# Performance work log

Measured on AMD Instinct MI355X. Metric: run time of the kernel, lower is better.

The kernel has to match this reference:

```python
import jax, jax.numpy as jnp
import numpy as np

DIM = 2048
N_HEADS = 16
HEAD_DIM = DIM // N_HEADS
B, S = 2, 2048


def apply_rotary(x, cos, sin):
    # x: [..., dim]; cos/sin broadcast to [..., dim//2]
    # even/odd interleaved rotation, matching the torch ::2 / 1::2 indexing
    xe = x[..., 0::2]
    xo = x[..., 1::2]
    oe = xe * cos - xo * sin
    oo = xo * cos + xe * sin
    return jnp.stack([oe, oo], axis=-1).reshape(x.shape)


def setup_inputs() -> dict:
    key = jax.random.key(0)
    ks = jax.random.split(key, 12)
    scale = 1.0 / np.sqrt(DIM)
    x = jax.random.normal(ks[0], (B, S, DIM), dtype=jnp.float32)
    cos = jax.random.normal(ks[1], (S, DIM // 2), dtype=jnp.float32)
    sin = jax.random.normal(ks[2], (S, DIM // 2), dtype=jnp.float32)
    mask = jnp.zeros((1, 1, S, S), dtype=jnp.float32)
    Wq = jax.random.normal(ks[3], (DIM, DIM), dtype=jnp.float32) * scale
    bq = jnp.zeros((DIM,), dtype=jnp.float32)
    Wk = jax.random.normal(ks[4], (DIM, DIM), dtype=jnp.float32) * scale
    bk = jnp.zeros((DIM,), dtype=jnp.float32)
    Wv = jax.random.normal(ks[5], (DIM, DIM), dtype=jnp.float32) * scale
    bv = jnp.zeros((DIM,), dtype=jnp.float32)
    Wo = jax.random.normal(ks[6], (DIM, DIM), dtype=jnp.float32) * scale
    bo = jnp.zeros((DIM,), dtype=jnp.float32)
    return {"x": x, "cos": cos, "sin": sin, "mask": mask,
            "Wq": Wq, "bq": bq, "Wk": Wk, "bk": bk,
            "Wv": Wv, "bv": bv, "Wo": Wo, "bo": bo}


def reference(x, cos, sin, mask, Wq, bq, Wk, bk, Wv, bv, Wo, bo):
    # Linear projections (torch nn.Linear: y = x @ W.T + b)
    q = jnp.einsum('bsd,ed->bse', x, Wq) + bq
    k = jnp.einsum('bsd,ed->bse', x, Wk) + bk
    v = jnp.einsum('bsd,ed->bse', x, Wv) + bv
    # RoPE on full dim, then split into heads (faithful to source ordering)
    q = apply_rotary(q, cos, sin).reshape(B, S, N_HEADS, HEAD_DIM)
    k = apply_rotary(k, cos, sin).reshape(B, S, N_HEADS, HEAD_DIM)
    v = v.reshape(B, S, N_HEADS, HEAD_DIM)
    scale = 1.0 / jnp.sqrt(jnp.float32(HEAD_DIM))
    attn = jnp.einsum('bqhd,bkhd->bhqk', q, k) * scale  # [B,H,S,S]
    attn = attn + mask
    attn = jax.nn.softmax(attn, axis=-1)
    out = jnp.einsum('bhqk,bkhd->bqhd', attn, v).reshape(B, S, DIM)
    return jnp.einsum('bsd,ed->bse', out, Wo) + bo
```

## Files before the change

kernel.cpp:

```cpp
#include <hip/hip_runtime.h>

#define DIM   2048
#define SLEN  2048
#define BATCH 2
#define NHEAD 16
#define HDIM  128
#define MROWS (BATCH*SLEN)

typedef __attribute__((ext_vector_type(8))) __bf16 bf16x8;
typedef __attribute__((ext_vector_type(4))) float  f32x4;
typedef __attribute__((ext_vector_type(8))) unsigned short u16x8;
typedef __attribute__((ext_vector_type(4))) unsigned short u16x4;

__device__ __forceinline__ unsigned short f2bf(float f) {
  union { float f; unsigned u; } v; v.f = f;
  unsigned r = v.u + 0x7FFFu + ((v.u >> 16) & 1u);
  return (unsigned short)(r >> 16);
}
__device__ __forceinline__ float bf2f(unsigned short h) {
  union { unsigned u; float f; } v; v.u = ((unsigned)h) << 16;
  return v.f;
}
__device__ __forceinline__ void gload16(const void* g, void* l) {
  __builtin_amdgcn_global_load_lds(
      (const __attribute__((address_space(1))) void*)g,
      (__attribute__((address_space(3))) void*)l, 16, 0, 0);
}

__global__ __launch_bounds__(256) void conv_f32_bf16(
    const float* __restrict__ in, unsigned short* __restrict__ out, int n4) {
  int t = blockIdx.x * 256 + threadIdx.x;
  if (t >= n4) return;
  f32x4 v = *(const f32x4*)(in + (size_t)t * 4);
  u16x4 o;
  o[0] = f2bf(v[0]); o[1] = f2bf(v[1]); o[2] = f2bf(v[2]); o[3] = f2bf(v[3]);
  *(u16x4*)(out + (size_t)t * 4) = o;
}

template<int OUT_MODE>
__global__ __launch_bounds__(256) void gemm_bt(
    const unsigned short* __restrict__ A,
    const unsigned short* __restrict__ Bw,
    const float* __restrict__ bias,
    void* __restrict__ Cout, int M, int N, int K)
{
  __shared__ __align__(16) unsigned short As[128][32];
  __shared__ __align__(16) unsigned short Bs[128][32];
  const int tid  = threadIdx.x;
  const int lane = tid & 63;
  const int wid  = tid >> 6;
  const int wr   = wid >> 1, wc = wid & 1;
  const int lrow = lane >> 4, lcol = lane & 15;
  const int row0 = blockIdx.x * 128, col0 = blockIdx.y * 128;

  f32x4 acc[4][4] = {};

  const unsigned short* Ablk = A  + (size_t)row0 * K;
  const unsigned short* Bblk = Bw + (size_t)col0 * K;
  char* AsB = (char*)&As[0][0];
  char* BsB = (char*)&Bs[0][0];

  for (int k0 = 0; k0 < K; k0 += 32) {
#pragma unroll
    for (int r = 0; r < 2; ++r) {
      int f = r * 256 + tid;
      gload16(Ablk + (size_t)(f >> 2) * K + k0 + (f & 3) * 8, AsB + (r * 256 + wid * 64) * 16);
      gload16(Bblk + (size_t)(f >> 2) * K + k0 + (f & 3) * 8, BsB + (r * 256 + wid * 64) * 16);
    }
    __syncthreads();
    bf16x8 af[4], bfv[4];
#pragma unroll
    for (int m = 0; m < 4; ++m)
      af[m] = *(const bf16x8*)&As[wr * 64 + m * 16 + lcol][lrow * 8];
#pragma unroll
    for (int n = 0; n < 4; ++n)
      bfv[n] = *(const bf16x8*)&Bs[wc * 64 + n * 16 + lcol][lrow * 8];
#pragma unroll
    for (int m = 0; m < 4; ++m)
#pragma unroll
      for (int n = 0; n < 4; ++n)
        acc[m][n] = __builtin_amdgcn_mfma_f32_16x16x32_bf16(af[m], bfv[n], acc[m][n], 0, 0, 0);
    __syncthreads();
  }

#pragma unroll
  for (int m = 0; m < 4; ++m) {
#pragma unroll
    for (int n = 0; n < 4; ++n) {
      int col = col0 + wc * 64 + n * 16 + lcol;
      float bv = bias[col];
      if (OUT_MODE == 2) {
        int row = row0 + wr * 64 + m * 16 + lrow * 4;
        u16x4 o;
#pragma unroll
        for (int j = 0; j < 4; ++j) o[j] = f2bf(acc[m][n][j] + bv);
        *(u16x4*)((unsigned short*)Cout +
                  ((size_t)((row >> 11) * DIM + col)) * SLEN + (row & (SLEN - 1))) = o;
      } else {
#pragma unroll
        for (int j = 0; j < 4; ++j) {
          int row = row0 + wr * 64 + m * 16 + lrow * 4 + j;
          float val = acc[m][n][j] + bv;
          if (OUT_MODE == 1) ((unsigned short*)Cout)[(size_t)row * N + col] = f2bf(val);
          else               ((float*)Cout)[(size_t)row * N + col] = val;
        }
      }
    }
  }
}

__global__ __launch_bounds__(256) void rope_inplace(
    unsigned short* __restrict__ q,
    const float* __restrict__ cosT, const float* __restrict__ sinT) {
  int t   = blockIdx.x * 256 + threadIdx.x;
  int row = t >> 8;
  int e0  = (t & 255) * 8;
  int s   = row & (SLEN - 1);
  unsigned short* p = q + (size_t)row * DIM + e0;
  u16x8 v = *(u16x8*)p;
  f32x4 c  = *(const f32x4*)(cosT + (size_t)s * (DIM / 2) + (e0 >> 1));
  f32x4 sn = *(const f32x4*)(sinT + (size_t)s * (DIM / 2) + (e0 >> 1));
#pragma unroll
  for (int i = 0; i < 4; ++i) {
    float xe = bf2f(v[2 * i]), xo = bf2f(v[2 * i + 1]);
    float oe = xe * c[i] - xo * sn[i];
    float oo = xo * c[i] + xe * sn[i];
    v[2 * i] = f2bf(oe); v[2 * i + 1] = f2bf(oo);
  }
  *(u16x8*)p = v;
}

__global__ __launch_bounds__(256) void attn_fwd(
    const unsigned short* __restrict__ Q,
    const unsigned short* __restrict__ Kg,
    const unsigned short* __restrict__ VtG,
    const float* __restrict__ mask,
    unsigned short* __restrict__ O)
{
  __shared__ __align__(16) unsigned short Ks[64][128];
  __shared__ __align__(16) unsigned short Vts[128][64];
  __shared__ __align__(16) unsigned short Ps[4][16][64];

  const int qt = blockIdx.x, h = blockIdx.y, b = blockIdx.z;
  const int tid = threadIdx.x, lane = tid & 63, wid = tid >> 6;
  const int lrow = lane >> 4, lcol = lane & 15;
  const int sx = (lcol & 7) << 4;
  const float scale = 0.08838834764831845f;

  const unsigned short* Qb  = Q  + ((size_t)(b * SLEN + qt * 64)) * DIM + h * HDIM;
  const unsigned short* Kb  = Kg + (size_t)(b * SLEN) * DIM + h * HDIM;
  const unsigned short* Vtb = VtG + ((size_t)(b * DIM + h * HDIM)) * SLEN;

  bf16x8 qf[4];
#pragma unroll
  for (int kk = 0; kk < 4; ++kk)
    qf[kk] = *(const bf16x8*)(Qb + (size_t)(wid * 16 + lcol) * DIM + kk * 32 + lrow * 8);

  float m_run[4], l_run[4];
  f32x4 acc_o[8] = {};
#pragma unroll
  for (int r = 0; r < 4; ++r) { m_run[r] = -1e30f; l_run[r] = 0.f; }

  char* KsB  = (char*)&Ks[0][0];
  char* VtsB = (char*)&Vts[0][0];
  char* PsB  = (char*)&Ps[0][0][0];

  for (int kt = 0; kt < SLEN / 64; ++kt) {
    __syncthreads();
#pragma unroll
    for (int r = 0; r < 4; ++r) {
      int L = r * 256 + wid * 64 + lane;
      int krow = L >> 4, kc = (L & 15) ^ (krow & 7);
      gload16(Kb + (size_t)(kt * 64 + krow) * DIM + kc * 8,
              KsB + (size_t)(r * 256 + wid * 64) * 16);
    }
#pragma unroll
    for (int r = 0; r < 4; ++r) {
      int L = r * 256 + wid * 64 + lane;
      int d = L >> 3, vc = (L & 7) ^ (d & 7);
      gload16(Vtb + (size_t)d * SLEN + kt * 64 + vc * 8,
              VtsB + (size_t)(r * 256 + wid * 64) * 16);
    }
    __syncthreads();

    f32x4 sacc[4] = {};
#pragma unroll
    for (int kn = 0; kn < 4; ++kn)
#pragma unroll
      for (int kk = 0; kk < 4; ++kk) {
        bf16x8 kf = *(const bf16x8*)(KsB + (size_t)(kn * 16 + lcol) * 256
                                         + ((kk * 64 + lrow * 16) ^ sx));
        sacc[kn] = __builtin_amdgcn_mfma_f32_16x16x32_bf16(qf[kk], kf, sacc[kn], 0, 0, 0);
      }

    int q0 = qt * 64 + wid * 16 + lrow * 4;
    float sv[4][4];
#pragma unroll
    for (int kn = 0; kn < 4; ++kn) {
      int kglob = kt * 64 + kn * 16 + lcol;
#pragma unroll
      for (int r = 0; r < 4; ++r)
        sv[kn][r] = sacc[kn][r] * scale + mask[(size_t)(q0 + r) * SLEN + kglob];
    }
    float alpha[4];
#pragma unroll
    for (int r = 0; r < 4; ++r) {
      float m0 = fmaxf(fmaxf(sv[0][r], sv[1][r]), fmaxf(sv[2][r], sv[3][r]));
#pragma unroll
      for (int off = 1; off < 16; off <<= 1) m0 = fmaxf(m0, __shfl_xor(m0, off, 64));
      float mt = fmaxf(m_run[r], m0);
      alpha[r] = __expf(m_run[r] - mt);
      m_run[r] = mt;
    }
    float pv[4][4];
#pragma unroll
    for (int r = 0; r < 4; ++r) {
      float rsum = 0.f;
#pragma unroll
      for (int kn = 0; kn < 4; ++kn) {
        float pe = __expf(sv[kn][r] - m_run[r]);
        pv[kn][r] = pe; rsum += pe;
      }
#pragma unroll
      for (int off = 1; off < 16; off <<= 1) rsum += __shfl_xor(rsum, off, 64);
      l_run[r] = l_run[r] * alpha[r] + rsum;
    }
#pragma unroll
    for (int d = 0; d < 8; ++d) {
      f32x4 t = acc_o[d];
      t[0] *= alpha[0]; t[1] *= alpha[1]; t[2] *= alpha[2]; t[3] *= alpha[3];
      acc_o[d] = t;
    }
#pragma unroll
    for (int kn = 0; kn < 4; ++kn)
#pragma unroll
      for (int r = 0; r < 4; ++r) {
        int prow = lrow * 4 + r;
        *(unsigned short*)(PsB + wid * 2048 + prow * 128
                           + ((kn * 32 + lcol * 2) ^ ((prow & 7) << 4))) = f2bf(pv[kn][r]);
      }

    bf16x8 pf[2];
#pragma unroll
    for (int ks = 0; ks < 2; ++ks)
      pf[ks] = *(const bf16x8*)(PsB + wid * 2048 + lcol * 128
                                + ((ks * 64 + lrow * 16) ^ sx));
#pragma unroll
    for (int d = 0; d < 8; ++d)
#pragma unroll
      for (int ks = 0; ks < 2; ++ks) {
        bf16x8 vf = *(const bf16x8*)(VtsB + (size_t)(d * 16 + lcol) * 128
                                          + ((ks * 64 + lrow * 16) ^ sx));
        acc_o[d] = __builtin_amdgcn_mfma_f32_16x16x32_bf16(pf[ks], vf, acc_o[d], 0, 0, 0);
      }
  }

  int orow0 = b * SLEN + qt * 64 + wid * 16 + lrow * 4;
#pragma unroll
  for (int d = 0; d < 8; ++d)
#pragma unroll
    for (int r = 0; r < 4; ++r) {
      float o = acc_o[d][r] / l_run[r];
      O[(size_t)(orow0 + r) * DIM + h * HDIM + d * 16 + lcol] = f2bf(o);
    }
}

extern "C" void kernel_launch(void* const* d_in, const int* in_sizes, int n_in,
                              void* d_out, int out_size, void* d_ws, size_t ws_size,
                              hipStream_t stream) {
  const float* x    = (const float*)d_in[0];
  const float* cosT = (const float*)d_in[1];
  const float* sinT = (const float*)d_in[2];
  const float* mask = (const float*)d_in[3];
  const float* Wq   = (const float*)d_in[4];
  const float* bq   = (const float*)d_in[5];
  const float* Wk   = (const float*)d_in[6];
  const float* bk   = (const float*)d_in[7];
  const float* Wv   = (const float*)d_in[8];
  const float* bv   = (const float*)d_in[9];
  const float* Wo   = (const float*)d_in[10];
  const float* bo   = (const float*)d_in[11];

  const size_t MB = 1u << 20;
  if (ws_size < 72 * MB) return;

  char* ws = (char*)d_ws;
  unsigned short* xb = (unsigned short*)(ws);
  unsigned short* qb = (unsigned short*)(ws + 16 * MB);
  unsigned short* kb = (unsigned short*)(ws + 32 * MB);
  unsigned short* Vt = (unsigned short*)(ws + 48 * MB);
  unsigned short* Wb = (unsigned short*)(ws + 64 * MB);
  unsigned short* Ob = xb;

  dim3 gGemm(MROWS / 128, DIM / 128);

  conv_f32_bf16<<<8192, 256, 0, stream>>>(x, xb, (MROWS * DIM) / 4);
  conv_f32_bf16<<<4096, 256, 0, stream>>>(Wq, Wb, (DIM * DIM) / 4);
  gemm_bt<1><<<gGemm, 256, 0, stream>>>(xb, Wb, bq, qb, MROWS, DIM, DIM);
  conv_f32_bf16<<<4096, 256, 0, stream>>>(Wk, Wb, (DIM * DIM) / 4);
  gemm_bt<1><<<gGemm, 256, 0, stream>>>(xb, Wb, bk, kb, MROWS, DIM, DIM);
  conv_f32_bf16<<<4096, 256, 0, stream>>>(Wv, Wb, (DIM * DIM) / 4);
  gemm_bt<2><<<gGemm, 256, 0, stream>>>(xb, Wb, bv, Vt, MROWS, DIM, DIM);
  rope_inplace<<<4096, 256, 0, stream>>>(qb, cosT, sinT);
  rope_inplace<<<4096, 256, 0, stream>>>(kb, cosT, sinT);
  attn_fwd<<<dim3(SLEN / 64, NHEAD, BATCH), 256, 0, stream>>>(qb, kb, Vt, mask, Ob);
  conv_f32_bf16<<<4096, 256, 0, stream>>>(Wo, Wb, (DIM * DIM) / 4);
  gemm_bt<0><<<gGemm, 256, 0, stream>>>(Ob, Wb, bo, d_out, MROWS, DIM, DIM);
}
```

Measured before the change: 450.7 us.

## Transpose score MFMA layout, fold scale into RoPE, lazy softmax rescaling

Swaps the MFMA operands for the QK^T product so each lane owns a single query row. This turns the softmax max and sum reductions into two cross-lane shuffles instead of four per row, and lets the mask be read as vectorized f32x4 loads. The 1/sqrt(d) scale moves into the Q RoPE kernel. The running-max rescale of the output accumulator is skipped unless some row's max rises by more than 8, trading a bounded growth of exp values for fewer multiplies. The P tile write layout is adjusted to match, and the final division becomes a reciprocal multiply.

```diff
diff --git a/kernel.cpp b/kernel.cpp
--- a/kernel.cpp
+++ b/kernel.cpp
@@ -111,7 +111,7 @@
 
 __global__ __launch_bounds__(256) void rope_inplace(
     unsigned short* __restrict__ q,
-    const float* __restrict__ cosT, const float* __restrict__ sinT) {
+    const float* __restrict__ cosT, const float* __restrict__ sinT, float scale) {
   int t   = blockIdx.x * 256 + threadIdx.x;
   int row = t >> 8;
   int e0  = (t & 255) * 8;
@@ -123,8 +123,8 @@
 #pragma unroll
   for (int i = 0; i < 4; ++i) {
     float xe = bf2f(v[2 * i]), xo = bf2f(v[2 * i + 1]);
-    float oe = xe * c[i] - xo * sn[i];
-    float oo = xo * c[i] + xe * sn[i];
+    float oe = (xe * c[i] - xo * sn[i]) * scale;
+    float oo = (xo * c[i] + xe * sn[i]) * scale;
     v[2 * i] = f2bf(oe); v[2 * i + 1] = f2bf(oo);
   }
   *(u16x8*)p = v;
@@ -145,21 +145,19 @@
   const int tid = threadIdx.x, lane = tid & 63, wid = tid >> 6;
   const int lrow = lane >> 4, lcol = lane & 15;
   const int sx = (lcol & 7) << 4;
-  const float scale = 0.08838834764831845f;
 
   const unsigned short* Qb  = Q  + ((size_t)(b * SLEN + qt * 64)) * DIM + h * HDIM;
   const unsigned short* Kb  = Kg + (size_t)(b * SLEN) * DIM + h * HDIM;
   const unsigned short* Vtb = VtG + ((size_t)(b * DIM + h * HDIM)) * SLEN;
+  const float* maskRow = mask + (size_t)(qt * 64 + wid * 16 + lcol) * SLEN;
 
   bf16x8 qf[4];
 #pragma unroll
   for (int kk = 0; kk < 4; ++kk)
     qf[kk] = *(const bf16x8*)(Qb + (size_t)(wid * 16 + lcol) * DIM + kk * 32 + lrow * 8);
 
-  float m_run[4], l_run[4];
+  float m_run = -1e30f, l_run = 0.f;
   f32x4 acc_o[8] = {};
-#pragma unroll
-  for (int r = 0; r < 4; ++r) { m_run[r] = -1e30f; l_run[r] = 0.f; }
 
   char* KsB  = (char*)&Ks[0][0];
   char* VtsB = (char*)&Vts[0][0];
@@ -190,55 +188,54 @@
       for (int kk = 0; kk < 4; ++kk) {
         bf16x8 kf = *(const bf16x8*)(KsB + (size_t)(kn * 16 + lcol) * 256
                                          + ((kk * 64 + lrow * 16) ^ sx));
-        sacc[kn] = __builtin_amdgcn_mfma_f32_16x16x32_bf16(qf[kk], kf, sacc[kn], 0, 0, 0);
+        sacc[kn] = __builtin_amdgcn_mfma_f32_16x16x32_bf16(kf, qf[kk], sacc[kn], 0, 0, 0);
       }
 
-    int q0 = qt * 64 + wid * 16 + lrow * 4;
-    float sv[4][4];
+    float sv[16];
 #pragma unroll
     for (int kn = 0; kn < 4; ++kn) {
-      int kglob = kt * 64 + kn * 16 + lcol;
+      f32x4 mv = *(const f32x4*)(maskRow + kt * 64 + kn * 16 + lrow * 4);
+#pragma unroll
+      for (int r = 0; r < 4; ++r) sv[kn * 4 + r] = sacc[kn][r] + mv[r];
+    }
+
+    float pmax = sv[0];
+#pragma unroll
+    for (int i = 1; i < 16; ++i) pmax = fmaxf(pmax, sv[i]);
+    pmax = fmaxf(pmax, __shfl_xor(pmax, 16, 64));
+    pmax = fmaxf(pmax, __shfl_xor(pmax, 32, 64));
+
+    if (!__all(pmax - m_run <= 8.0f)) {
+      float mnew = fmaxf(m_run, pmax);
+      float alpha = __expf(m_run - mnew);
+      m_run = mnew;
+      l_run *= alpha;
+      float ar[4];
+#pragma unroll
+      for (int r = 0; r < 4; ++r) ar[r] = __shfl(alpha, lrow * 4 + r, 64);
+#pragma unroll
+      for (int d = 0; d < 8; ++d) {
+        f32x4 t = acc_o[d];
+#pragma unroll
+        for (int r = 0; r < 4; ++r) t[r] *= ar[r];
+        acc_o[d] = t;
+      }
+    }
+
+    float pv[16];
+    float rsum = 0.f;
+#pragma unroll
+    for (int i = 0; i < 16; ++i) { float pe = __expf(sv[i] - m_run); pv[i] = pe; rsum += pe; }
+    rsum += __shfl_xor(rsum, 16, 64);
+    rsum += __shfl_xor(rsum, 32, 64);
+    l_run += rsum;
+
+#pragma unroll
+    for (int kn = 0; kn < 4; ++kn)
 #pragma unroll
       for (int r = 0; r < 4; ++r)
-        sv[kn][r] = sacc[kn][r] * scale + mask[(size_t)(q0 + r) * SLEN + kglob];
-    }
-    float alpha[4];
-#pragma unroll
-    for (int r = 0; r < 4; ++r) {
-      float m0 = fmaxf(fmaxf(sv[0][r], sv[1][r]), fmaxf(sv[2][r], sv[3][r]));
-#pragma unroll
-      for (int off = 1; off < 16; off <<= 1) m0 = fmaxf(m0, __shfl_xor(m0, off, 64));
-      float mt = fmaxf(m_run[r], m0);
-      alpha[r] = __expf(m_run[r] - mt);
-      m_run[r] = mt;
-    }
-    float pv[4][4];
-#pragma unroll
-    for (int r = 0; r < 4; ++r) {
-      float rsum = 0.f;
-#pragma unroll
-      for (int kn = 0; kn < 4; ++kn) {
-        float pe = __expf(sv[kn][r] - m_run[r]);
-        pv[kn][r] = pe; rsum += pe;
-      }
-#pragma unroll
-      for (int off = 1; off < 16; off <<= 1) rsum += __shfl_xor(rsum, off, 64);
-      l_run[r] = l_run[r] * alpha[r] + rsum;
-    }
-#pragma unroll
-    for (int d = 0; d < 8; ++d) {
-      f32x4 t = acc_o[d];
-      t[0] *= alpha[0]; t[1] *= alpha[1]; t[2] *= alpha[2]; t[3] *= alpha[3];
-      acc_o[d] = t;
-    }
-#pragma unroll
-    for (int kn = 0; kn < 4; ++kn)
-#pragma unroll
-      for (int r = 0; r < 4; ++r) {
-        int prow = lrow * 4 + r;
-        *(unsigned short*)(PsB + wid * 2048 + prow * 128
-                           + ((kn * 32 + lcol * 2) ^ ((prow & 7) << 4))) = f2bf(pv[kn][r]);
-      }
+        *(unsigned short*)(PsB + wid * 2048 + lcol * 128
+                           + ((kn * 32 + (lrow * 4 + r) * 2) ^ sx)) = f2bf(pv[kn * 4 + r]);
 
     bf16x8 pf[2];
 #pragma unroll
@@ -255,12 +252,15 @@
       }
   }
 
+  float linv[4];
+#pragma unroll
+  for (int r = 0; r < 4; ++r) linv[r] = 1.0f / __shfl(l_run, lrow * 4 + r, 64);
   int orow0 = b * SLEN + qt * 64 + wid * 16 + lrow * 4;
 #pragma unroll
   for (int d = 0; d < 8; ++d)
 #pragma unroll
     for (int r = 0; r < 4; ++r) {
-      float o = acc_o[d][r] / l_run[r];
+      float o = acc_o[d][r] * linv[r];
       O[(size_t)(orow0 + r) * DIM + h * HDIM + d * 16 + lcol] = f2bf(o);
     }
 }
@@ -293,6 +293,7 @@
   unsigned short* Ob = xb;
 
   dim3 gGemm(MROWS / 128, DIM / 128);
+  const float scale = 0.08838834764831845f;
 
   conv_f32_bf16<<<8192, 256, 0, stream>>>(x, xb, (MROWS * DIM) / 4);
   conv_f32_bf16<<<4096, 256, 0, stream>>>(Wq, Wb, (DIM * DIM) / 4);
@@ -301,8 +302,8 @@
   gemm_bt<1><<<gGemm, 256, 0, stream>>>(xb, Wb, bk, kb, MROWS, DIM, DIM);
   conv_f32_bf16<<<4096, 256, 0, stream>>>(Wv, Wb, (DIM * DIM) / 4);
   gemm_bt<2><<<gGemm, 256, 0, stream>>>(xb, Wb, bv, Vt, MROWS, DIM, DIM);
-  rope_inplace<<<4096, 256, 0, stream>>>(qb, cosT, sinT);
-  rope_inplace<<<4096, 256, 0, stream>>>(kb, cosT, sinT);
+  rope_inplace<<<4096, 256, 0, stream>>>(qb, cosT, sinT, scale);
+  rope_inplace<<<4096, 256, 0, stream>>>(kb, cosT, sinT, 1.0f);
   attn_fwd<<<dim3(SLEN / 64, NHEAD, BATCH), 256, 0, stream>>>(qb, kb, Vt, mask, Ob);
   conv_f32_bf16<<<4096, 256, 0, stream>>>(Wo, Wb, (DIM * DIM) / 4);
   gemm_bt<0><<<gGemm, 256, 0, stream>>>(Ob, Wb, bo, d_out, MROWS, DIM, DIM);
```

Result: faster. 434.8 us (-3.5%).
